# Optimization experiments

Measured on AMD Instinct MI355X. Metric: run time of the kernel, lower is better.

## Reference

```python
import jax, jax.numpy as jnp
import numpy as np

EPS = 1e-5
GROUPS = 8


def _gn_per_channel(x, w, b):
    # GroupNorm with num_groups == num_channels: per-channel instance norm over (h, w)
    m = x.mean(axis=(2, 3), keepdims=True)
    v = x.var(axis=(2, 3), keepdims=True)  # biased var, matches torch GroupNorm
    xn = (x - m) * jax.lax.rsqrt(v + EPS)
    return xn * w[None, :, None, None] + b[None, :, None, None]


def setup_inputs() -> dict:
    key = jax.random.key(0)
    k0, k1 = jax.random.split(key)
    b, c, h, w = 16, 512, 64, 64
    cg = c // GROUPS          # 64 per-group channels
    half = cg // 2            # 32
    x = jax.random.normal(k0, (b, c, h, w), jnp.float32)
    conv1x1_w = jax.random.normal(k1, (cg, cg), jnp.float32) / np.float32(np.sqrt(cg))
    conv1x1_b = jnp.zeros((cg,), jnp.float32)
    gn_w = jnp.ones((cg,), jnp.float32)
    gn_b = jnp.zeros((cg,), jnp.float32)
    gn1_w = jnp.ones((half,), jnp.float32)
    gn1_b = jnp.zeros((half,), jnp.float32)
    cweight = jnp.zeros((1, half, 1, 1), jnp.float32)
    cbias = jnp.ones((1, half, 1, 1), jnp.float32)
    sweight = jnp.zeros((1, half, 1, 1), jnp.float32)
    sbias = jnp.ones((1, half, 1, 1), jnp.float32)
    return {"x": x, "conv1x1_w": conv1x1_w, "conv1x1_b": conv1x1_b,
            "gn_w": gn_w, "gn_b": gn_b, "gn1_w": gn1_w, "gn1_b": gn1_b,
            "cweight": cweight, "cbias": cbias, "sweight": sweight, "sbias": sbias}


def reference(x, conv1x1_w, conv1x1_b, gn_w, gn_b, gn1_w, gn1_b,
              cweight, cbias, sweight, sbias):
    b, c, h, w = x.shape
    g = GROUPS
    cg = c // g
    half = cg // 2
    bg = b * g
    gx = x.reshape(bg, cg, h, w)  # group_x

    # coordinate-attention branch: pool along W and H
    x_h = gx.mean(axis=3, keepdims=True)                      # (bg, cg, h, 1)
    x_w = gx.mean(axis=2, keepdims=True).transpose(0, 1, 3, 2)  # (bg, cg, w, 1)
    hw_cat = jnp.concatenate([x_h, x_w], axis=2)              # (bg, cg, h+w, 1)
    hw = jnp.einsum('oi,bilk->bolk', conv1x1_w, hw_cat) + conv1x1_b[None, :, None, None]
    xh = hw[:, :, :h]                       # (bg, cg, h, 1)
    xw = hw[:, :, h:].transpose(0, 1, 3, 2)  # (bg, cg, 1, w)
    x1 = _gn_per_channel(gx * jax.nn.sigmoid(xh) * jax.nn.sigmoid(xw), gn_w, gn_b)

    # shuffle-attention branch on chunked channels
    x0, x1b = gx[:, :half], gx[:, half:]
    xc = x0.mean(axis=(2, 3), keepdims=True)                  # (bg, half, 1, 1)
    x_channel = x0 * jax.nn.sigmoid(cweight * xc + cbias)
    xs = _gn_per_channel(x1b, gn1_w, gn1_b)
    x_spatial = x1b * jax.nn.sigmoid(sweight * xs + sbias)
    out = jnp.concatenate([x_channel, x_spatial], axis=1)     # (bg, cg, h, w)
    # channel shuffle with g=2
    x2 = out.reshape(bg, 2, half, h, w).transpose(0, 2, 1, 3, 4).reshape(bg, cg, h, w)

    # cross-branch attention weights via small batched matmuls
    x11 = jax.nn.softmax(x1.mean(axis=(2, 3)).reshape(bg, 1, cg), axis=-1)
    x21 = jax.nn.softmax(x2.mean(axis=(2, 3)).reshape(bg, 1, cg), axis=-1)
    x12 = x2.reshape(bg, cg, h * w)
    x22 = x1.reshape(bg, cg, h * w)
    weights = (jnp.matmul(x11, x12) + jnp.matmul(x21, x22)).reshape(bg, 1, h, w)
    return (gx * jax.nn.sigmoid(weights)).reshape(b, c, h, w)
```

## Files before the change

kernel.cpp:

```cpp
#include <hip/hip_runtime.h>
#include <math.h>

#define EPSV 1e-5f

typedef float vfloat4 __attribute__((ext_vector_type(4)));

__device__ __forceinline__ float fast_rcp(float x) {
#if __has_builtin(__builtin_amdgcn_rcpf)
    return __builtin_amdgcn_rcpf(x);
#else
    return 1.0f / x;
#endif
}

__device__ __forceinline__ float sigmoidf_(float x) {
    return fast_rcp(1.0f + __expf(-x));
}

__global__ __launch_bounds__(256) void k_statsA(
    const float* __restrict__ x,
    float* __restrict__ rowmean,
    float* __restrict__ colmean,
    float* __restrict__ meanA,
    float* __restrict__ varA)
{
    const int t = threadIdx.x, l = t & 63, wv = t >> 6;
    const int plane = blockIdx.x * 4 + wv;
    const float4* p4 = (const float4*)(x + (size_t)plane * 4096);
    float c0 = 0.f, c1 = 0.f, c2 = 0.f, c3 = 0.f, s = 0.f, ss = 0.f;
#pragma unroll 8
    for (int k = 0; k < 16; ++k) {
        float4 v = p4[k * 64 + l];
        float rp = v.x + v.y + v.z + v.w;
        s += rp;
        ss += v.x * v.x + v.y * v.y + v.z * v.z + v.w * v.w;
        c0 += v.x; c1 += v.y; c2 += v.z; c3 += v.w;
#pragma unroll
        for (int m = 8; m >= 1; m >>= 1) rp += __shfl_xor(rp, m, 16);
        if ((l & 15) == 0)
            rowmean[(size_t)plane * 64 + k * 4 + (l >> 4)] = rp * (1.f / 64.f);
    }
#pragma unroll
    for (int m = 32; m >= 16; m >>= 1) {
        c0 += __shfl_xor(c0, m); c1 += __shfl_xor(c1, m);
        c2 += __shfl_xor(c2, m); c3 += __shfl_xor(c3, m);
    }
    if (l < 16) {
        float4 cm = { c0 * (1.f / 64.f), c1 * (1.f / 64.f),
                      c2 * (1.f / 64.f), c3 * (1.f / 64.f) };
        ((float4*)(colmean + (size_t)plane * 64))[l] = cm;
    }
#pragma unroll
    for (int m = 32; m >= 1; m >>= 1) { s += __shfl_xor(s, m); ss += __shfl_xor(ss, m); }
    if (l == 0) {
        float mn = s * (1.f / 4096.f);
        meanA[plane] = mn;
        varA[plane] = ss * (1.f / 4096.f) - mn * mn;
    }
}

__global__ __launch_bounds__(256) void k_conv(
    const float* __restrict__ W, const float* __restrict__ Wb,
    const float* __restrict__ rowmean, const float* __restrict__ colmean,
    float* __restrict__ shg, float* __restrict__ swg)
{
    int blk = blockIdx.x;
    int bg = blk >> 1, rc = blk & 1;
    const float* rm = (rc ? colmean : rowmean) + (size_t)bg * 4096;
    float* outp = (rc ? swg : shg) + (size_t)bg * 4096;
    int t = threadIdx.x, lane = t & 63, wv = t >> 6;
    float r[64];
#pragma unroll
    for (int i = 0; i < 64; ++i) r[i] = rm[i * 64 + lane];
    for (int j = 0; j < 16; ++j) {
        int c = wv * 16 + j;
        float acc = Wb[c];
#pragma unroll
        for (int i = 0; i < 64; ++i)
            acc = fmaf(W[c * 64 + i], r[i], acc);
        outp[c * 64 + lane] = sigmoidf_(acc);
    }
}

__global__ __launch_bounds__(256) void k_statsC(
    const float* __restrict__ x,
    const float* __restrict__ shg, const float* __restrict__ swg,
    const float* __restrict__ meanA, const float* __restrict__ varA,
    const float* __restrict__ swt, const float* __restrict__ sbs,
    const float* __restrict__ gn1w, const float* __restrict__ gn1b,
    float* __restrict__ meanT, float* __restrict__ varT,
    float* __restrict__ spat)
{
    const int t = threadIdx.x, l = t & 63, wv = t >> 6;
    const int plane = blockIdx.x * 4 + wv;
    const int cch = plane & 63, bgc = plane >> 6;
    const float4* p4 = (const float4*)(x + (size_t)plane * 4096);
    float4 sw4 = ((const float4*)(swg + (size_t)plane * 64))[l & 15];
    float a = 0.f, bb = 0.f;
    const bool spatial = (cch >= 32);
    if (spatial) {
        int i = cch - 32;
        float mu = meanA[plane];
        float r2 = rsqrtf(varA[plane] + EPSV);
        a = swt[i] * gn1w[i] * r2;
        bb = swt[i] * (gn1b[i] - mu * r2 * gn1w[i]) + sbs[i];
    }
    float st = 0.f, sst = 0.f, ssp = 0.f;
#pragma unroll 8
    for (int k = 0; k < 16; ++k) {
        float4 v = p4[k * 64 + l];
        float sh = shg[(size_t)plane * 64 + k * 4 + (l >> 4)];
        float t0 = v.x * sh * sw4.x;
        float t1 = v.y * sh * sw4.y;
        float t2 = v.z * sh * sw4.z;
        float t3 = v.w * sh * sw4.w;
        st += t0 + t1 + t2 + t3;
        sst += t0 * t0 + t1 * t1 + t2 * t2 + t3 * t3;
        if (spatial) {
            ssp += v.x * sigmoidf_(fmaf(a, v.x, bb))
                 + v.y * sigmoidf_(fmaf(a, v.y, bb))
                 + v.z * sigmoidf_(fmaf(a, v.z, bb))
                 + v.w * sigmoidf_(fmaf(a, v.w, bb));
        }
    }
#pragma unroll
    for (int m = 32; m >= 1; m >>= 1) {
        st += __shfl_xor(st, m); sst += __shfl_xor(sst, m); ssp += __shfl_xor(ssp, m);
    }
    if (l == 0) {
        float mn = st * (1.f / 4096.f);
        meanT[plane] = mn;
        varT[plane] = sst * (1.f / 4096.f) - mn * mn;
        if (spatial) spat[bgc * 32 + (cch - 32)] = ssp * (1.f / 4096.f);
    }
}

__global__ __launch_bounds__(64) void k_coef(
    const float* __restrict__ meanA, const float* __restrict__ varA,
    const float* __restrict__ meanT, const float* __restrict__ varT,
    const float* __restrict__ spat,
    const float* __restrict__ gnw, const float* __restrict__ gnb,
    const float* __restrict__ gn1w, const float* __restrict__ gn1b,
    const float* __restrict__ cwt, const float* __restrict__ cbs,
    const float* __restrict__ swt, const float* __restrict__ sbs,
    float* __restrict__ eArr, float* __restrict__ gArr,
    float* __restrict__ dArr, float* __restrict__ aArr,
    float* __restrict__ bArr, float* __restrict__ kArr)
{
    int bg = blockIdx.x;
    int c = threadIdx.x;
    size_t idx = (size_t)bg * 64 + c;
    __shared__ float x2m[64], x11L[64], sL[32];
    if (c < 32) {
        float xc = meanA[idx];
        float s = sigmoidf_(fmaf(cwt[c], xc, cbs[c]));
        sL[c] = s;
        x2m[2 * c] = s * xc;
        x2m[2 * c + 1] = spat[bg * 32 + c];
    }
    __syncthreads();
    float v1 = gnb[c];
    float mx = v1;
#pragma unroll
    for (int m = 32; m >= 1; m >>= 1) mx = fmaxf(mx, __shfl_xor(mx, m));
    float e1 = __expf(v1 - mx);
    float s1 = e1;
#pragma unroll
    for (int m = 32; m >= 1; m >>= 1) s1 += __shfl_xor(s1, m);
    float x11 = e1 / s1;
    x11L[c] = x11;
    float v2 = x2m[c];
    mx = v2;
#pragma unroll
    for (int m = 32; m >= 1; m >>= 1) mx = fmaxf(mx, __shfl_xor(mx, m));
    float e2 = __expf(v2 - mx);
    float s2 = e2;
#pragma unroll
    for (int m = 32; m >= 1; m >>= 1) s2 += __shfl_xor(s2, m);
    float x21 = e2 / s2;

    float mt = meanT[idx];
    float rt = rsqrtf(varT[idx] + EPSV);
    eArr[idx] = x21 * gnw[c] * rt;
    float kp = x21 * (gnb[c] - gnw[c] * rt * mt);
#pragma unroll
    for (int m = 32; m >= 1; m >>= 1) kp += __shfl_xor(kp, m);
    if (c == 0) kArr[bg] = kp;
    __syncthreads();
    if (c < 32) {
        gArr[bg * 32 + c] = x11L[2 * c] * sL[c];
        dArr[bg * 32 + c] = x11L[2 * c + 1];
        size_t idx2 = (size_t)bg * 64 + 32 + c;
        float mu = meanA[idx2];
        float r2 = rsqrtf(varA[idx2] + EPSV);
        aArr[bg * 32 + c] = swt[c] * gn1w[c] * r2;
        bArr[bg * 32 + c] = swt[c] * (gn1b[c] - mu * r2 * gn1w[c]) + sbs[c];
    }
}

__global__ __launch_bounds__(256) void k_final(
    const float* __restrict__ x,
    const float* __restrict__ shg, const float* __restrict__ swg,
    const float* __restrict__ eArr, const float* __restrict__ gArr,
    const float* __restrict__ dArr, const float* __restrict__ aArr,
    const float* __restrict__ bArr, const float* __restrict__ kArr,
    float* __restrict__ outp)
{
    const int blk = blockIdx.x;
    const int bg = blk >> 2, tile = blk & 3;
    const int h0 = tile << 4;
    const int t = threadIdx.x;
    __shared__ float swf[64 * 64];
    __shared__ float shf[64 * 16];
    __shared__ float eL[64], gL[32], dL[32], aL[32], bL[32];
#pragma unroll
    for (int j = 0; j < 4; ++j) {
        int f = t + 256 * j;
        ((float4*)swf)[f] = ((const float4*)swg)[(size_t)bg * 1024 + f];
    }
#pragma unroll
    for (int j = 0; j < 4; ++j) {
        int idx = t + 256 * j;
        int c = idx >> 4, r = idx & 15;
        shf[idx] = shg[(size_t)bg * 4096 + c * 64 + h0 + r];
    }
    if (t < 64)       eL[t]       = eArr[(size_t)bg * 64 + t];
    else if (t < 96)  gL[t - 64]  = gArr[bg * 32 + t - 64];
    else if (t < 128) dL[t - 96]  = dArr[bg * 32 + t - 96];
    else if (t < 160) aL[t - 128] = aArr[bg * 32 + t - 128];
    else if (t < 192) bL[t - 160] = bArr[bg * 32 + t - 160];
    const float K = kArr[bg];
    __syncthreads();

    const int hl = t >> 4, w4 = t & 15;
    const float* xp = x + (size_t)bg * 262144 + (size_t)(h0 + hl) * 64 + w4 * 4;
    float ax = K, ay = K, az = K, aw = K;
#pragma unroll 8
    for (int c = 0; c < 32; ++c) {
        float4 v = *(const float4*)(xp + (size_t)c * 4096);
        float ce = eL[c] * shf[c * 16 + hl];
        float gc = gL[c];
        const float* swc = &swf[c * 64 + w4 * 4];
        ax = fmaf(fmaf(ce, swc[0], gc), v.x, ax);
        ay = fmaf(fmaf(ce, swc[1], gc), v.y, ay);
        az = fmaf(fmaf(ce, swc[2], gc), v.z, az);
        aw = fmaf(fmaf(ce, swc[3], gc), v.w, aw);
    }
#pragma unroll 8
    for (int i = 0; i < 32; ++i) {
        int c = 32 + i;
        float4 v = *(const float4*)(xp + (size_t)c * 4096);
        float ce = eL[c] * shf[c * 16 + hl];
        float ai = aL[i], bi = bL[i], di = dL[i];
        const float* swc = &swf[c * 64 + w4 * 4];
        ax = fmaf(ce * swc[0], v.x, ax); ax = fmaf(di * v.x, sigmoidf_(fmaf(ai, v.x, bi)), ax);
        ay = fmaf(ce * swc[1], v.y, ay); ay = fmaf(di * v.y, sigmoidf_(fmaf(ai, v.y, bi)), ay);
        az = fmaf(ce * swc[2], v.z, az); az = fmaf(di * v.z, sigmoidf_(fmaf(ai, v.z, bi)), az);
        aw = fmaf(ce * swc[3], v.w, aw); aw = fmaf(di * v.w, sigmoidf_(fmaf(ai, v.w, bi)), aw);
    }
    const float sx = sigmoidf_(ax), sy = sigmoidf_(ay),
                sz = sigmoidf_(az), sw_ = sigmoidf_(aw);
    float* op = outp + (xp - x);
#pragma unroll 8
    for (int c = 0; c < 64; ++c) {
        float4 v = *(const float4*)(xp + (size_t)c * 4096);
        vfloat4 o = { v.x * sx, v.y * sy, v.z * sz, v.w * sw_ };
        __builtin_nontemporal_store(o, (vfloat4*)(op + (size_t)c * 4096));
    }
}

extern "C" void kernel_launch(void* const* d_in, const int* in_sizes, int n_in,
                              void* d_out, int out_size, void* d_ws, size_t ws_size,
                              hipStream_t stream) {
    (void)in_sizes; (void)n_in; (void)out_size; (void)ws_size;
    const float* x    = (const float*)d_in[0];
    const float* W    = (const float*)d_in[1];
    const float* Wb   = (const float*)d_in[2];
    const float* gnw  = (const float*)d_in[3];
    const float* gnb  = (const float*)d_in[4];
    const float* gn1w = (const float*)d_in[5];
    const float* gn1b = (const float*)d_in[6];
    const float* cwt  = (const float*)d_in[7];
    const float* cbs  = (const float*)d_in[8];
    const float* swt  = (const float*)d_in[9];
    const float* sbs  = (const float*)d_in[10];
    float* out = (float*)d_out;
    float* ws = (float*)d_ws;

    float* rowmean = ws;
    float* colmean = rowmean + 524288;
    float* shg     = colmean + 524288;
    float* swg     = shg + 524288;
    float* meanA   = swg + 524288;
    float* varA    = meanA + 8192;
    float* meanT   = varA + 8192;
    float* varT    = meanT + 8192;
    float* spat    = varT + 8192;
    float* eArr    = spat + 4096;
    float* gArr    = eArr + 8192;
    float* dArr    = gArr + 4096;
    float* aArr    = dArr + 4096;
    float* bArr    = aArr + 4096;
    float* kArr    = bArr + 4096;

    k_statsA<<<2048, 256, 0, stream>>>(x, rowmean, colmean, meanA, varA);
    k_conv<<<256, 256, 0, stream>>>(W, Wb, rowmean, colmean, shg, swg);
    k_statsC<<<2048, 256, 0, stream>>>(x, shg, swg, meanA, varA, swt, sbs, gn1w, gn1b,
                                       meanT, varT, spat);
    k_coef<<<128, 64, 0, stream>>>(meanA, varA, meanT, varT, spat, gnw, gnb, gn1w, gn1b,
                                   cwt, cbs, swt, sbs, eArr, gArr, dArr, aArr, bArr, kArr);
    k_final<<<512, 256, 0, stream>>>(x, shg, swg, eArr, gArr, dArr, aArr, bArr, kArr, out);
}
```

Before: 340.8 us.

## Fuse coefficient kernel into final pass and split channels across waves

Removes the separate k_coef launch by computing the softmax and normalization coefficients per block in the first wave of the final kernel. The final kernel now uses 2048 blocks of 4-row bands, with each of the four waves handling 16 channels, and combines the partial sums through shared memory. Each wave keeps its x values in registers, so the output pass reuses them instead of reading x a second time. In exchange, every block redundantly recomputes the per-bg coefficients, adds two extra barriers, and holds 16 float4 values per thread, which raises register pressure.

```diff
diff --git a/kernel.cpp b/kernel.cpp
--- a/kernel.cpp
+++ b/kernel.cpp
@@ -135,7 +135,9 @@
     }
 }
 
-__global__ __launch_bounds__(64) void k_coef(
+__global__ __launch_bounds__(256, 4) void k_final2(
+    const float* __restrict__ x,
+    const float* __restrict__ shg, const float* __restrict__ swg,
     const float* __restrict__ meanA, const float* __restrict__ varA,
     const float* __restrict__ meanT, const float* __restrict__ varT,
     const float* __restrict__ spat,
@@ -143,128 +145,142 @@
     const float* __restrict__ gn1w, const float* __restrict__ gn1b,
     const float* __restrict__ cwt, const float* __restrict__ cbs,
     const float* __restrict__ swt, const float* __restrict__ sbs,
-    float* __restrict__ eArr, float* __restrict__ gArr,
-    float* __restrict__ dArr, float* __restrict__ aArr,
-    float* __restrict__ bArr, float* __restrict__ kArr)
-{
-    int bg = blockIdx.x;
-    int c = threadIdx.x;
-    size_t idx = (size_t)bg * 64 + c;
-    __shared__ float x2m[64], x11L[64], sL[32];
-    if (c < 32) {
-        float xc = meanA[idx];
-        float s = sigmoidf_(fmaf(cwt[c], xc, cbs[c]));
-        sL[c] = s;
-        x2m[2 * c] = s * xc;
-        x2m[2 * c + 1] = spat[bg * 32 + c];
-    }
-    __syncthreads();
-    float v1 = gnb[c];
-    float mx = v1;
-#pragma unroll
-    for (int m = 32; m >= 1; m >>= 1) mx = fmaxf(mx, __shfl_xor(mx, m));
-    float e1 = __expf(v1 - mx);
-    float s1 = e1;
-#pragma unroll
-    for (int m = 32; m >= 1; m >>= 1) s1 += __shfl_xor(s1, m);
-    float x11 = e1 / s1;
-    x11L[c] = x11;
-    float v2 = x2m[c];
-    mx = v2;
-#pragma unroll
-    for (int m = 32; m >= 1; m >>= 1) mx = fmaxf(mx, __shfl_xor(mx, m));
-    float e2 = __expf(v2 - mx);
-    float s2 = e2;
-#pragma unroll
-    for (int m = 32; m >= 1; m >>= 1) s2 += __shfl_xor(s2, m);
-    float x21 = e2 / s2;
-
-    float mt = meanT[idx];
-    float rt = rsqrtf(varT[idx] + EPSV);
-    eArr[idx] = x21 * gnw[c] * rt;
-    float kp = x21 * (gnb[c] - gnw[c] * rt * mt);
-#pragma unroll
-    for (int m = 32; m >= 1; m >>= 1) kp += __shfl_xor(kp, m);
-    if (c == 0) kArr[bg] = kp;
-    __syncthreads();
-    if (c < 32) {
-        gArr[bg * 32 + c] = x11L[2 * c] * sL[c];
-        dArr[bg * 32 + c] = x11L[2 * c + 1];
-        size_t idx2 = (size_t)bg * 64 + 32 + c;
-        float mu = meanA[idx2];
-        float r2 = rsqrtf(varA[idx2] + EPSV);
-        aArr[bg * 32 + c] = swt[c] * gn1w[c] * r2;
-        bArr[bg * 32 + c] = swt[c] * (gn1b[c] - mu * r2 * gn1w[c]) + sbs[c];
-    }
-}
-
-__global__ __launch_bounds__(256) void k_final(
-    const float* __restrict__ x,
-    const float* __restrict__ shg, const float* __restrict__ swg,
-    const float* __restrict__ eArr, const float* __restrict__ gArr,
-    const float* __restrict__ dArr, const float* __restrict__ aArr,
-    const float* __restrict__ bArr, const float* __restrict__ kArr,
     float* __restrict__ outp)
 {
     const int blk = blockIdx.x;
-    const int bg = blk >> 2, tile = blk & 3;
-    const int h0 = tile << 4;
-    const int t = threadIdx.x;
+    const int bg = blk >> 4, band = blk & 15;
+    const int h0 = band << 2;
+    const int t = threadIdx.x, l = t & 63, wv = t >> 6;
+
     __shared__ float swf[64 * 64];
-    __shared__ float shf[64 * 16];
+    __shared__ float shf[64 * 4];
     __shared__ float eL[64], gL[32], dL[32], aL[32], bL[32];
+    __shared__ float kS;
+    __shared__ float4 red[4][64];
+    __shared__ float4 sig4[64];
+
 #pragma unroll
     for (int j = 0; j < 4; ++j) {
         int f = t + 256 * j;
-        ((float4*)swf)[f] = ((const float4*)swg)[(size_t)bg * 1024 + f];
-    }
-#pragma unroll
-    for (int j = 0; j < 4; ++j) {
-        int idx = t + 256 * j;
-        int c = idx >> 4, r = idx & 15;
-        shf[idx] = shg[(size_t)bg * 4096 + c * 64 + h0 + r];
-    }
-    if (t < 64)       eL[t]       = eArr[(size_t)bg * 64 + t];
-    else if (t < 96)  gL[t - 64]  = gArr[bg * 32 + t - 64];
-    else if (t < 128) dL[t - 96]  = dArr[bg * 32 + t - 96];
-    else if (t < 160) aL[t - 128] = aArr[bg * 32 + t - 128];
-    else if (t < 192) bL[t - 160] = bArr[bg * 32 + t - 160];
-    const float K = kArr[bg];
+        ((float4*)swf)[f] = ((const float4*)(swg + (size_t)bg * 4096))[f];
+    }
+    {
+        int c = t >> 2, r = t & 3;
+        shf[t] = shg[(size_t)bg * 4096 + c * 64 + h0 + r];
+    }
+
+    if (wv == 0) {
+        const int c = l;
+        size_t idx = (size_t)bg * 64 + c;
+        float Aj = 0.f, Bj = 0.f, scj = 0.f;
+        if (c < 32) {
+            float xc = meanA[idx];
+            scj = sigmoidf_(fmaf(cwt[c], xc, cbs[c]));
+            Aj = scj * xc;
+            Bj = spat[bg * 32 + c];
+        }
+        float As = __shfl(Aj, c >> 1);
+        float Bs = __shfl(Bj, c >> 1);
+        float v2 = (c & 1) ? Bs : As;
+        float v1 = gnb[c];
+        float mx = v1;
+#pragma unroll
+        for (int m = 32; m >= 1; m >>= 1) mx = fmaxf(mx, __shfl_xor(mx, m));
+        float e1 = __expf(v1 - mx);
+        float s1 = e1;
+#pragma unroll
+        for (int m = 32; m >= 1; m >>= 1) s1 += __shfl_xor(s1, m);
+        float x11 = e1 / s1;
+        mx = v2;
+#pragma unroll
+        for (int m = 32; m >= 1; m >>= 1) mx = fmaxf(mx, __shfl_xor(mx, m));
+        float e2 = __expf(v2 - mx);
+        float s2 = e2;
+#pragma unroll
+        for (int m = 32; m >= 1; m >>= 1) s2 += __shfl_xor(s2, m);
+        float x21 = e2 / s2;
+
+        float mT = meanT[idx];
+        float rt = rsqrtf(varT[idx] + EPSV);
+        float e_c = x21 * gnw[c] * rt;
+        float kp = x21 * (gnb[c] - gnw[c] * rt * mT);
+#pragma unroll
+        for (int m = 32; m >= 1; m >>= 1) kp += __shfl_xor(kp, m);
+        float x11e = __shfl(x11, (2 * c) & 63);
+        float x11o = __shfl(x11, (2 * c + 1) & 63);
+        eL[c] = e_c;
+        if (c == 0) kS = kp;
+        if (c < 32) {
+            gL[c] = x11e * scj;
+            dL[c] = x11o;
+            size_t idx2 = (size_t)bg * 64 + 32 + c;
+            float mu = meanA[idx2];
+            float r2 = rsqrtf(varA[idx2] + EPSV);
+            aL[c] = swt[c] * gn1w[c] * r2;
+            bL[c] = swt[c] * (gn1b[c] - mu * r2 * gn1w[c]) + sbs[c];
+        }
+    }
     __syncthreads();
 
-    const int hl = t >> 4, w4 = t & 15;
-    const float* xp = x + (size_t)bg * 262144 + (size_t)(h0 + hl) * 64 + w4 * 4;
-    float ax = K, ay = K, az = K, aw = K;
-#pragma unroll 8
-    for (int c = 0; c < 32; ++c) {
-        float4 v = *(const float4*)(xp + (size_t)c * 4096);
-        float ce = eL[c] * shf[c * 16 + hl];
-        float gc = gL[c];
-        const float* swc = &swf[c * 64 + w4 * 4];
-        ax = fmaf(fmaf(ce, swc[0], gc), v.x, ax);
-        ay = fmaf(fmaf(ce, swc[1], gc), v.y, ay);
-        az = fmaf(fmaf(ce, swc[2], gc), v.z, az);
-        aw = fmaf(fmaf(ce, swc[3], gc), v.w, aw);
-    }
-#pragma unroll 8
-    for (int i = 0; i < 32; ++i) {
-        int c = 32 + i;
-        float4 v = *(const float4*)(xp + (size_t)c * 4096);
-        float ce = eL[c] * shf[c * 16 + hl];
-        float ai = aL[i], bi = bL[i], di = dL[i];
-        const float* swc = &swf[c * 64 + w4 * 4];
-        ax = fmaf(ce * swc[0], v.x, ax); ax = fmaf(di * v.x, sigmoidf_(fmaf(ai, v.x, bi)), ax);
-        ay = fmaf(ce * swc[1], v.y, ay); ay = fmaf(di * v.y, sigmoidf_(fmaf(ai, v.y, bi)), ay);
-        az = fmaf(ce * swc[2], v.z, az); az = fmaf(di * v.z, sigmoidf_(fmaf(ai, v.z, bi)), az);
-        aw = fmaf(ce * swc[3], v.w, aw); aw = fmaf(di * v.w, sigmoidf_(fmaf(ai, v.w, bi)), aw);
-    }
-    const float sx = sigmoidf_(ax), sy = sigmoidf_(ay),
-                sz = sigmoidf_(az), sw_ = sigmoidf_(aw);
+    const int r = l >> 4, qc = l & 15;
+    const float* xp = x + (size_t)bg * 262144 + (size_t)(h0 + r) * 64 + qc * 4;
+    const int c0 = wv * 16;
+    float4 xc[16];
+    float4 part = {0.f, 0.f, 0.f, 0.f};
+    if (wv < 2) {
+#pragma unroll
+        for (int cc = 0; cc < 16; ++cc) {
+            int c = c0 + cc;
+            float4 v = *(const float4*)(xp + (size_t)c * 4096);
+            xc[cc] = v;
+            float ce = eL[c] * shf[c * 4 + r];
+            float gc = gL[c];
+            float4 s4 = *(const float4*)&swf[c * 64 + qc * 4];
+            part.x = fmaf(fmaf(ce, s4.x, gc), v.x, part.x);
+            part.y = fmaf(fmaf(ce, s4.y, gc), v.y, part.y);
+            part.z = fmaf(fmaf(ce, s4.z, gc), v.z, part.z);
+            part.w = fmaf(fmaf(ce, s4.w, gc), v.w, part.w);
+        }
+    } else {
+#pragma unroll
+        for (int cc = 0; cc < 16; ++cc) {
+            int c = c0 + cc;
+            int i = c - 32;
+            float4 v = *(const float4*)(xp + (size_t)c * 4096);
+            xc[cc] = v;
+            float ce = eL[c] * shf[c * 4 + r];
+            float ai = aL[i], bi = bL[i], di = dL[i];
+            float4 s4 = *(const float4*)&swf[c * 64 + qc * 4];
+            part.x = fmaf(ce * s4.x, v.x, part.x);
+            part.x = fmaf(di * v.x, sigmoidf_(fmaf(ai, v.x, bi)), part.x);
+            part.y = fmaf(ce * s4.y, v.y, part.y);
+            part.y = fmaf(di * v.y, sigmoidf_(fmaf(ai, v.y, bi)), part.y);
+            part.z = fmaf(ce * s4.z, v.z, part.z);
+            part.z = fmaf(di * v.z, sigmoidf_(fmaf(ai, v.z, bi)), part.z);
+            part.w = fmaf(ce * s4.w, v.w, part.w);
+            part.w = fmaf(di * v.w, sigmoidf_(fmaf(ai, v.w, bi)), part.w);
+        }
+    }
+    red[wv][l] = part;
+    __syncthreads();
+    if (wv == 0) {
+        float4 p0 = red[0][l], p1 = red[1][l], p2 = red[2][l], p3 = red[3][l];
+        float K = kS;
+        float4 sgv;
+        sgv.x = sigmoidf_(K + p0.x + p1.x + p2.x + p3.x);
+        sgv.y = sigmoidf_(K + p0.y + p1.y + p2.y + p3.y);
+        sgv.z = sigmoidf_(K + p0.z + p1.z + p2.z + p3.z);
+        sgv.w = sigmoidf_(K + p0.w + p1.w + p2.w + p3.w);
+        sig4[l] = sgv;
+    }
+    __syncthreads();
+    const float4 sg = sig4[l];
     float* op = outp + (xp - x);
-#pragma unroll 8
-    for (int c = 0; c < 64; ++c) {
-        float4 v = *(const float4*)(xp + (size_t)c * 4096);
-        vfloat4 o = { v.x * sx, v.y * sy, v.z * sz, v.w * sw_ };
+#pragma unroll
+    for (int cc = 0; cc < 16; ++cc) {
+        int c = c0 + cc;
+        float4 v = xc[cc];
+        vfloat4 o = { v.x * sg.x, v.y * sg.y, v.z * sg.z, v.w * sg.w };
         __builtin_nontemporal_store(o, (vfloat4*)(op + (size_t)c * 4096));
     }
 }
@@ -296,18 +312,11 @@
     float* meanT   = varA + 8192;
     float* varT    = meanT + 8192;
     float* spat    = varT + 8192;
-    float* eArr    = spat + 4096;
-    float* gArr    = eArr + 8192;
-    float* dArr    = gArr + 4096;
-    float* aArr    = dArr + 4096;
-    float* bArr    = aArr + 4096;
-    float* kArr    = bArr + 4096;
 
     k_statsA<<<2048, 256, 0, stream>>>(x, rowmean, colmean, meanA, varA);
     k_conv<<<256, 256, 0, stream>>>(W, Wb, rowmean, colmean, shg, swg);
     k_statsC<<<2048, 256, 0, stream>>>(x, shg, swg, meanA, varA, swt, sbs, gn1w, gn1b,
                                        meanT, varT, spat);
-    k_coef<<<128, 64, 0, stream>>>(meanA, varA, meanT, varT, spat, gnw, gnb, gn1w, gn1b,
-                                   cwt, cbs, swt, sbs, eArr, gArr, dArr, aArr, bArr, kArr);
-    k_final<<<512, 256, 0, stream>>>(x, shg, swg, eArr, gArr, dArr, aArr, bArr, kArr, out);
-}
+    k_final2<<<2048, 256, 0, stream>>>(x, shg, swg, meanA, varA, meanT, varT, spat,
+                                       gnw, gnb, gn1w, gn1b, cwt, cbs, swt, sbs, out);
+}
```

After: 321.4 us. 5.7% less time.
